# Optimization experiments

Measured on AMD Instinct MI355X. Metric: run time of the kernel, lower is better.

Reference implementation:

```python
import jax, jax.numpy as jnp
import numpy as np

M = 16
N = 16
T = 100
H1 = (M + N) * 10 * 8          # 2560
H2 = (M * N) * 1 * 4           # 1024
HID = (N * N + M * M) * 10     # 5120, GRU hidden dim


def setup_inputs() -> dict:
    key = jax.random.key(0)
    ks = jax.random.split(key, 16)
    def rn(k, shape, scale=1.0):
        return (jax.random.normal(k, shape, dtype=jnp.float32) * scale)
    inp = {}
    inp["y"] = rn(ks[0], (N, T))
    # scale F so spectral radius ~0.8 -> stable over T steps
    inp["F"] = rn(ks[1], (M, M), 0.2)
    inp["H"] = rn(ks[2], (N, M))
    inp["m1_0"] = rn(ks[3], (M, 1))
    inp["h0"] = rn(ks[4], (HID,))
    D_in, D_out = M + N, M * N
    inp["W1"] = rn(ks[5], (H1, D_in), 1.0 / np.sqrt(D_in))
    inp["b1"] = jnp.zeros((H1,), jnp.float32)
    inp["W_ih"] = rn(ks[6], (3 * HID, H1), 1.0 / np.sqrt(H1))
    inp["b_ih"] = jnp.zeros((3 * HID,), jnp.float32)
    inp["W_hh"] = rn(ks[7], (3 * HID, HID), 1.0 / np.sqrt(HID))
    inp["b_hh"] = jnp.zeros((3 * HID,), jnp.float32)
    inp["W2"] = rn(ks[8], (H2, HID), 1.0 / np.sqrt(HID))
    inp["b2"] = jnp.zeros((H2,), jnp.float32)
    inp["W3"] = rn(ks[9], (D_out, H2), 1.0 / np.sqrt(H2))
    inp["b3"] = jnp.zeros((D_out,), jnp.float32)
    return inp


def _l2_normalize(x):
    # torch F.normalize(p=2, eps=1e-12): x / max(||x||_2, eps)
    return x / jnp.maximum(jnp.linalg.norm(x), 1e-12)


def reference(y, F, H, m1_0, h0, W1, b1, W_ih, b_ih, W_hh, b_hh, W2, b2, W3, b3):
    m, n = F.shape[0], H.shape[0]

    def gru_cell(x, h):
        gi = W_ih @ x + b_ih            # [3*HID]
        gh = W_hh @ h + b_hh            # [3*HID]
        i_r, i_z, i_n = jnp.split(gi, 3)
        h_r, h_z, h_n = jnp.split(gh, 3)
        r = jax.nn.sigmoid(i_r + h_r)
        z = jax.nn.sigmoid(i_z + h_z)
        nn_ = jnp.tanh(i_n + r * h_n)
        return (1.0 - z) * nn_ + z * h

    def step(carry, y_t):
        post, sp_post, h = carry
        # step_prior
        m1x_prior = F @ post            # [m,1]
        m1y = H @ m1x_prior             # [n,1]
        sp_prior = F @ sp_post          # [m,1]
        obs0 = H @ sp_prior             # [n,1]
        # step_KGain_est
        d_norm = _l2_normalize((post - sp_post)[:, 0])
        y_norm = _l2_normalize(y_t - obs0[:, 0])
        kin = jnp.concatenate([d_norm, y_norm])  # [m+n]
        l1 = jax.nn.relu(W1 @ kin + b1)
        h_new = gru_cell(l1, h)
        l2 = jax.nn.relu(W2 @ h_new + b2)
        KG = (W3 @ l2 + b3).reshape(m, n)
        # innovation update
        dy = y_t[:, None] - m1y         # [n,1]
        post_new = m1x_prior + KG @ dy  # [m,1]
        return (post_new, sp_prior, h_new), post_new[:, 0]

    (_, _, _), xs = jax.lax.scan(step, (m1_0, m1_0, h0), y.T)
    return xs.T                         # [m,T]
```

## Files before the change

kernel.cpp:

```cpp
#include <hip/hip_runtime.h>
#include <math.h>

#define Tt  100
#define H1  2560
#define HID 5120
#define H2  1024

enum {
  OFF_POST = 0,
  OFF_SP   = 16,
  OFF_M1X  = 32,
  OFF_M1Y  = 48,
  OFF_SPR  = 64,
  OFF_KIN  = 80,
  OFF_L1   = 112,
  OFF_L2   = 2672,
  OFF_KG   = 3696,
  OFF_HA   = 3952,
  OFF_HB   = 9072,
};

__global__ void k_init(const float* __restrict__ m1_0, const float* __restrict__ h0,
                       float* __restrict__ ws) {
  int i = blockIdx.x * blockDim.x + threadIdx.x;
  if (i < 16) { ws[OFF_POST + i] = m1_0[i]; ws[OFF_SP + i] = m1_0[i]; }
  if (i < HID) ws[OFF_HA + i] = h0[i];
}

__global__ void k_small(const float* __restrict__ Fm, const float* __restrict__ Hm,
                        const float* __restrict__ y, float* __restrict__ ws,
                        float* __restrict__ out, int t, int do_F) {
  __shared__ float s_post[16], s_sp[16], s_m1x[16], s_spr[16], s_d[16], s_yv[16], s_dy[16];
  const int tid = threadIdx.x;
  float* post = ws + OFF_POST;
  float* sp   = ws + OFF_SP;
  float* m1x  = ws + OFF_M1X;
  float* m1y  = ws + OFF_M1Y;
  float* spr  = ws + OFF_SPR;
  float* kin  = ws + OFF_KIN;
  const float* KG = ws + OFF_KG;

  if (do_F) {
    if (tid < 16) s_dy[tid] = y[tid * Tt + (t - 1)] - m1y[tid];
    __syncthreads();
    if (tid < 16) {
      float acc = m1x[tid];
      #pragma unroll
      for (int j = 0; j < 16; j++) acc = fmaf(KG[tid * 16 + j], s_dy[j], acc);
      post[tid] = acc; s_post[tid] = acc;
      out[tid * Tt + (t - 1)] = acc;
      float sv = spr[tid];
      sp[tid] = sv; s_sp[tid] = sv;
    }
    __syncthreads();
  } else {
    if (tid < 16) { s_post[tid] = post[tid]; s_sp[tid] = sp[tid]; }
    __syncthreads();
  }
  if (t >= Tt) return;

  if (tid < 16) {
    float a = 0.f, b = 0.f;
    #pragma unroll
    for (int j = 0; j < 16; j++) {
      a = fmaf(Fm[tid * 16 + j], s_post[j], a);
      b = fmaf(Fm[tid * 16 + j], s_sp[j], b);
    }
    s_m1x[tid] = a; s_spr[tid] = b;
    m1x[tid] = a; spr[tid] = b;
  }
  __syncthreads();
  if (tid < 16) {
    float my = 0.f, ob = 0.f;
    #pragma unroll
    for (int j = 0; j < 16; j++) {
      my = fmaf(Hm[tid * 16 + j], s_m1x[j], my);
      ob = fmaf(Hm[tid * 16 + j], s_spr[j], ob);
    }
    m1y[tid] = my;
    s_yv[tid] = y[tid * Tt + t] - ob;
    s_d[tid] = s_post[tid] - s_sp[tid];
  }
  __syncthreads();
  if (tid < 16) {
    float nd = 0.f, ny = 0.f;
    #pragma unroll
    for (int j = 0; j < 16; j++) { nd += s_d[j] * s_d[j]; ny += s_yv[j] * s_yv[j]; }
    nd = fmaxf(sqrtf(nd), 1e-12f);
    ny = fmaxf(sqrtf(ny), 1e-12f);
    kin[tid]      = s_d[tid] / nd;
    kin[16 + tid] = s_yv[tid] / ny;
  }
}

__global__ void k_l1(const float* __restrict__ W1, const float* __restrict__ b1,
                     const float* __restrict__ kin, float* __restrict__ l1) {
  __shared__ float s_kin[32];
  const int tid = threadIdx.x;
  const int r = blockIdx.x * 256 + tid;
  if (tid < 32) s_kin[tid] = kin[tid];
  __syncthreads();
  const float4* row = (const float4*)(W1 + (size_t)r * 32);
  float acc = b1[r];
  #pragma unroll
  for (int j = 0; j < 8; j++) {
    float4 w = row[j];
    acc = fmaf(w.x, s_kin[4 * j + 0], acc);
    acc = fmaf(w.y, s_kin[4 * j + 1], acc);
    acc = fmaf(w.z, s_kin[4 * j + 2], acc);
    acc = fmaf(w.w, s_kin[4 * j + 3], acc);
  }
  l1[r] = fmaxf(acc, 0.f);
}

__device__ __forceinline__ float block_reduce_256(float v, float* sdata) {
  const int tid = threadIdx.x;
  #pragma unroll
  for (int off = 32; off > 0; off >>= 1) v += __shfl_down(v, off, 64);
  __syncthreads();
  if ((tid & 63) == 0) sdata[tid >> 6] = v;
  __syncthreads();
  float r = (tid < 4) ? sdata[tid] : 0.f;
  r += __shfl_down(r, 2, 64);
  r += __shfl_down(r, 1, 64);
  return r;
}

__global__ void k_gru(const float* __restrict__ W_ih, const float* __restrict__ b_ih,
                      const float* __restrict__ W_hh, const float* __restrict__ b_hh,
                      const float* __restrict__ l1, const float* __restrict__ h_in,
                      float* __restrict__ h_out) {
  const int i = blockIdx.x;
  const int tid = threadIdx.x;
  __shared__ float sdata[4];
  const float4* l1v = (const float4*)l1;
  const float4* hv  = (const float4*)h_in;
  float p[6];
  #pragma unroll
  for (int g = 0; g < 3; g++) {
    const float4* row = (const float4*)(W_ih + (size_t)(i + g * HID) * H1);
    float acc = 0.f;
    for (int j = tid; j < H1 / 4; j += 256) {
      float4 w = row[j], x = l1v[j];
      acc = fmaf(w.x, x.x, fmaf(w.y, x.y, fmaf(w.z, x.z, fmaf(w.w, x.w, acc))));
    }
    p[g] = acc;
  }
  #pragma unroll
  for (int g = 0; g < 3; g++) {
    const float4* row = (const float4*)(W_hh + (size_t)(i + g * HID) * HID);
    float acc = 0.f;
    for (int j = tid; j < HID / 4; j += 256) {
      float4 w = row[j], x = hv[j];
      acc = fmaf(w.x, x.x, fmaf(w.y, x.y, fmaf(w.z, x.z, fmaf(w.w, x.w, acc))));
    }
    p[3 + g] = acc;
  }
  float s[6];
  #pragma unroll
  for (int k = 0; k < 6; k++) s[k] = block_reduce_256(p[k], sdata);
  if (tid == 0) {
    float ir = s[0] + b_ih[i], iz = s[1] + b_ih[i + HID], inn = s[2] + b_ih[i + 2 * HID];
    float hr = s[3] + b_hh[i], hz = s[4] + b_hh[i + HID], hn  = s[5] + b_hh[i + 2 * HID];
    float r = 1.f / (1.f + expf(-(ir + hr)));
    float z = 1.f / (1.f + expf(-(iz + hz)));
    float nn = tanhf(inn + r * hn);
    h_out[i] = (1.f - z) * nn + z * h_in[i];
  }
}

__global__ void k_l2(const float* __restrict__ W2, const float* __restrict__ b2,
                     const float* __restrict__ h, float* __restrict__ l2) {
  const int j = blockIdx.x;
  const int tid = threadIdx.x;
  __shared__ float sdata[4];
  const float4* row = (const float4*)(W2 + (size_t)j * HID);
  const float4* xv  = (const float4*)h;
  float acc = 0.f;
  for (int k = tid; k < HID / 4; k += 256) {
    float4 w = row[k], x = xv[k];
    acc = fmaf(w.x, x.x, fmaf(w.y, x.y, fmaf(w.z, x.z, fmaf(w.w, x.w, acc))));
  }
  float s = block_reduce_256(acc, sdata);
  if (tid == 0) l2[j] = fmaxf(s + b2[j], 0.f);
}

__global__ void k_kg(const float* __restrict__ W3, const float* __restrict__ b3,
                     const float* __restrict__ l2, float* __restrict__ KG) {
  const int k = blockIdx.x;
  const int tid = threadIdx.x;
  const float4* row = (const float4*)(W3 + (size_t)k * H2);
  const float4* xv  = (const float4*)l2;
  float acc = 0.f;
  for (int j = tid; j < H2 / 4; j += 64) {
    float4 w = row[j], x = xv[j];
    acc = fmaf(w.x, x.x, fmaf(w.y, x.y, fmaf(w.z, x.z, fmaf(w.w, x.w, acc))));
  }
  #pragma unroll
  for (int off = 32; off > 0; off >>= 1) acc += __shfl_down(acc, off, 64);
  if (tid == 0) KG[k] = acc + b3[k];
}

extern "C" void kernel_launch(void* const* d_in, const int* in_sizes, int n_in,
                              void* d_out, int out_size, void* d_ws, size_t ws_size,
                              hipStream_t stream) {
  const float* y    = (const float*)d_in[0];
  const float* Fm   = (const float*)d_in[1];
  const float* Hm   = (const float*)d_in[2];
  const float* m1_0 = (const float*)d_in[3];
  const float* h0   = (const float*)d_in[4];
  const float* W1   = (const float*)d_in[5];
  const float* b1   = (const float*)d_in[6];
  const float* W_ih = (const float*)d_in[7];
  const float* b_ih = (const float*)d_in[8];
  const float* W_hh = (const float*)d_in[9];
  const float* b_hh = (const float*)d_in[10];
  const float* W2   = (const float*)d_in[11];
  const float* b2   = (const float*)d_in[12];
  const float* W3   = (const float*)d_in[13];
  const float* b3   = (const float*)d_in[14];
  float* out = (float*)d_out;
  float* ws  = (float*)d_ws;

  k_init<<<(HID + 255) / 256, 256, 0, stream>>>(m1_0, h0, ws);

  for (int t = 0; t < Tt; t++) {
    k_small<<<1, 64, 0, stream>>>(Fm, Hm, y, ws, out, t, t > 0 ? 1 : 0);
    k_l1<<<H1 / 256, 256, 0, stream>>>(W1, b1, ws + OFF_KIN, ws + OFF_L1);
    const float* h_in = ws + ((t & 1) ? OFF_HB : OFF_HA);
    float* h_out      = ws + ((t & 1) ? OFF_HA : OFF_HB);
    k_gru<<<HID, 256, 0, stream>>>(W_ih, b_ih, W_hh, b_hh, ws + OFF_L1, h_in, h_out);
    k_l2<<<H2, 256, 0, stream>>>(W2, b2, h_out, ws + OFF_L2);
    k_kg<<<256, 64, 0, stream>>>(W3, b3, ws + OFF_L2, ws + OFF_KG);
  }
  k_small<<<1, 64, 0, stream>>>(Fm, Hm, y, ws, out, Tt, 1);
}
```

Before: 10.84 ms.

## Replace per-timestep kernel launches with single persistent kernel using atomic flag barriers

Folds the 100-step loop of five kernel launches into one persistent kernel of 1024 blocks. The blocks synchronise through atomic epoch counters and flags in workspace, and each block handles five GRU rows. The W_hh matvec is issued before waiting for l1, so it overlaps with block 0's serial Kalman and layer-1 work, and weight streams use nontemporal loads. The aim is to remove launch overhead and inter-kernel gaps. In exchange, correctness depends on all 1024 blocks being co-resident to avoid deadlock, and the spin-waits carry a bounded timeout.

```diff
diff --git a/kernel.cpp b/kernel.cpp
--- a/kernel.cpp
+++ b/kernel.cpp
@@ -5,200 +5,303 @@
 #define H1  2560
 #define HID 5120
 #define H2  1024
-
-enum {
-  OFF_POST = 0,
-  OFF_SP   = 16,
-  OFF_M1X  = 32,
-  OFF_M1Y  = 48,
-  OFF_SPR  = 64,
-  OFF_KIN  = 80,
-  OFF_L1   = 112,
-  OFF_L2   = 2672,
-  OFF_KG   = 3696,
-  OFF_HA   = 3952,
-  OFF_HB   = 9072,
-};
-
-__global__ void k_init(const float* __restrict__ m1_0, const float* __restrict__ h0,
-                       float* __restrict__ ws) {
-  int i = blockIdx.x * blockDim.x + threadIdx.x;
-  if (i < 16) { ws[OFF_POST + i] = m1_0[i]; ws[OFF_SP + i] = m1_0[i]; }
-  if (i < HID) ws[OFF_HA + i] = h0[i];
-}
-
-__global__ void k_small(const float* __restrict__ Fm, const float* __restrict__ Hm,
-                        const float* __restrict__ y, float* __restrict__ ws,
-                        float* __restrict__ out, int t, int do_F) {
-  __shared__ float s_post[16], s_sp[16], s_m1x[16], s_spr[16], s_d[16], s_yv[16], s_dy[16];
+#define NB  1024
+#define GPB 5
+
+typedef float v4 __attribute__((ext_vector_type(4)));
+
+#define FI_HEP   0
+#define FI_L1EP  16
+#define FI_L2EP  32
+#define FI_KGEP  48
+#define FI_HCNT  64
+#define FI_L2CNT 80
+#define FI_KGCNT 96
+
+#define OFF_M1X 128
+#define OFF_M1Y 144
+#define OFF_SPR 160
+#define OFF_KG  208
+#define OFF_L2  464
+#define OFF_L1  1488
+#define OFF_HB0 4048
+#define OFF_HB1 9168
+
+__device__ __forceinline__ void wait_ge(int* p, int v) {
+  if (threadIdx.x == 0) {
+    for (long it = 0; it < 10000000L; ++it) {
+      if (__hip_atomic_load(p, __ATOMIC_RELAXED, __HIP_MEMORY_SCOPE_AGENT) >= v) break;
+      __builtin_amdgcn_s_sleep(8);
+    }
+  }
+  __syncthreads();
+  __builtin_amdgcn_fence(__ATOMIC_ACQUIRE, "agent");
+}
+
+__device__ __forceinline__ void arrive(int* cnt, int* ep, int target, int epval) {
+  if (threadIdx.x == 0) {
+    __builtin_amdgcn_fence(__ATOMIC_RELEASE, "agent");
+    int c = __hip_atomic_fetch_add(cnt, 1, __ATOMIC_RELAXED, __HIP_MEMORY_SCOPE_AGENT);
+    if (c == target - 1) {
+      __builtin_amdgcn_fence(__ATOMIC_ACQUIRE, "agent");
+      __hip_atomic_store(ep, epval, __ATOMIC_RELEASE, __HIP_MEMORY_SCOPE_AGENT);
+    }
+  }
+}
+
+__device__ __forceinline__ float dot4(v4 w, v4 x, float acc) {
+  return fmaf(w.x, x.x, fmaf(w.y, x.y, fmaf(w.z, x.z, fmaf(w.w, x.w, acc))));
+}
+
+__global__ void k_pre(const float* __restrict__ m1_0, const float* __restrict__ h0,
+                      const float* __restrict__ y, const float* __restrict__ Fm,
+                      const float* __restrict__ Hm, const float* __restrict__ W1,
+                      const float* __restrict__ b1, float* __restrict__ ws) {
   const int tid = threadIdx.x;
-  float* post = ws + OFF_POST;
-  float* sp   = ws + OFF_SP;
-  float* m1x  = ws + OFF_M1X;
-  float* m1y  = ws + OFF_M1Y;
-  float* spr  = ws + OFF_SPR;
-  float* kin  = ws + OFF_KIN;
-  const float* KG = ws + OFF_KG;
-
-  if (do_F) {
-    if (tid < 16) s_dy[tid] = y[tid * Tt + (t - 1)] - m1y[tid];
-    __syncthreads();
+  __shared__ float s_m1x[16], s_kin[32];
+  __shared__ float s_ny;
+  for (int i = tid; i < HID; i += 256) ws[OFF_HB1 + i] = h0[i];
+  if (tid < 16) {
+    float a = 0.f;
+    #pragma unroll
+    for (int j = 0; j < 16; j++) a = fmaf(Fm[tid * 16 + j], m1_0[j], a);
+    s_m1x[tid] = a;
+  }
+  __syncthreads();
+  if (tid < 16) {
+    float my = 0.f;
+    #pragma unroll
+    for (int j = 0; j < 16; j++) my = fmaf(Hm[tid * 16 + j], s_m1x[j], my);
+    ws[OFF_M1X + tid] = s_m1x[tid];
+    ws[OFF_M1Y + tid] = my;
+    ws[OFF_SPR + tid] = s_m1x[tid];
+    s_kin[16 + tid] = y[tid * Tt + 0] - my;
+  }
+  __syncthreads();
+  if (tid == 0) {
+    float ny = 0.f;
+    #pragma unroll
+    for (int j = 0; j < 16; j++) ny += s_kin[16 + j] * s_kin[16 + j];
+    s_ny = fmaxf(sqrtf(ny), 1e-12f);
+  }
+  __syncthreads();
+  if (tid < 16) {
+    s_kin[tid] = 0.f;
+    s_kin[16 + tid] = s_kin[16 + tid] / s_ny;
+  }
+  __syncthreads();
+  for (int r = tid; r < H1; r += 256) {
+    const v4* row = (const v4*)(W1 + (size_t)r * 32);
+    float acc = b1[r];
+    #pragma unroll
+    for (int j = 0; j < 8; j++) {
+      v4 w = row[j];
+      acc = fmaf(w.x, s_kin[4 * j], fmaf(w.y, s_kin[4 * j + 1],
+            fmaf(w.z, s_kin[4 * j + 2], fmaf(w.w, s_kin[4 * j + 3], acc))));
+    }
+    ws[OFF_L1 + r] = fmaxf(acc, 0.f);
+  }
+  __syncthreads();
+  if (tid == 0) ((int*)ws)[FI_L1EP] = 1;
+}
+
+__launch_bounds__(256, 4)
+__global__ void k_persist(const float* __restrict__ y, const float* __restrict__ Fm,
+                          const float* __restrict__ Hm,
+                          const float* __restrict__ W1, const float* __restrict__ b1,
+                          const float* __restrict__ W_ih, const float* __restrict__ b_ih,
+                          const float* __restrict__ W_hh, const float* __restrict__ b_hh,
+                          const float* __restrict__ W2, const float* __restrict__ b2,
+                          const float* __restrict__ W3, const float* __restrict__ b3,
+                          float* __restrict__ out, float* __restrict__ ws) {
+  const int b = blockIdx.x, tid = threadIdx.x;
+  int* flags = (int*)ws;
+  float* l1  = ws + OFF_L1;
+  float* l2v = ws + OFF_L2;
+  float* KGg = ws + OFF_KG;
+
+  __shared__ float red[4][32];
+  __shared__ float s_m1x[16], s_m1y[16], s_spr[16], s_post[16], s_sp[16];
+  __shared__ float s_dy[16], s_d[16], s_yv[16], s_kin[32], s_nrm[2];
+
+  if (b == 0) {
     if (tid < 16) {
-      float acc = m1x[tid];
+      s_m1x[tid] = ws[OFF_M1X + tid];
+      s_m1y[tid] = ws[OFF_M1Y + tid];
+      s_spr[tid] = ws[OFF_SPR + tid];
+    }
+    __syncthreads();
+  }
+
+  for (int t = 0; t < Tt; ++t) {
+    wait_ge(flags + FI_HEP, t);
+    const float* hp = ws + ((t & 1) ? OFF_HB0 : OFF_HB1);
+    float*       hc = ws + ((t & 1) ? OFF_HB1 : OFF_HB0);
+    const v4* hp4 = (const v4*)hp;
+
+    float pv[30];
+    #pragma unroll
+    for (int k = 0; k < GPB; ++k) {
+      const int i = b + k * NB;
       #pragma unroll
-      for (int j = 0; j < 16; j++) acc = fmaf(KG[tid * 16 + j], s_dy[j], acc);
-      post[tid] = acc; s_post[tid] = acc;
-      out[tid * Tt + (t - 1)] = acc;
-      float sv = spr[tid];
-      sp[tid] = sv; s_sp[tid] = sv;
-    }
-    __syncthreads();
-  } else {
-    if (tid < 16) { s_post[tid] = post[tid]; s_sp[tid] = sp[tid]; }
-    __syncthreads();
-  }
-  if (t >= Tt) return;
-
-  if (tid < 16) {
-    float a = 0.f, b = 0.f;
-    #pragma unroll
-    for (int j = 0; j < 16; j++) {
-      a = fmaf(Fm[tid * 16 + j], s_post[j], a);
-      b = fmaf(Fm[tid * 16 + j], s_sp[j], b);
-    }
-    s_m1x[tid] = a; s_spr[tid] = b;
-    m1x[tid] = a; spr[tid] = b;
-  }
-  __syncthreads();
-  if (tid < 16) {
-    float my = 0.f, ob = 0.f;
-    #pragma unroll
-    for (int j = 0; j < 16; j++) {
-      my = fmaf(Hm[tid * 16 + j], s_m1x[j], my);
-      ob = fmaf(Hm[tid * 16 + j], s_spr[j], ob);
-    }
-    m1y[tid] = my;
-    s_yv[tid] = y[tid * Tt + t] - ob;
-    s_d[tid] = s_post[tid] - s_sp[tid];
-  }
-  __syncthreads();
-  if (tid < 16) {
-    float nd = 0.f, ny = 0.f;
-    #pragma unroll
-    for (int j = 0; j < 16; j++) { nd += s_d[j] * s_d[j]; ny += s_yv[j] * s_yv[j]; }
-    nd = fmaxf(sqrtf(nd), 1e-12f);
-    ny = fmaxf(sqrtf(ny), 1e-12f);
-    kin[tid]      = s_d[tid] / nd;
-    kin[16 + tid] = s_yv[tid] / ny;
-  }
-}
-
-__global__ void k_l1(const float* __restrict__ W1, const float* __restrict__ b1,
-                     const float* __restrict__ kin, float* __restrict__ l1) {
-  __shared__ float s_kin[32];
-  const int tid = threadIdx.x;
-  const int r = blockIdx.x * 256 + tid;
-  if (tid < 32) s_kin[tid] = kin[tid];
-  __syncthreads();
-  const float4* row = (const float4*)(W1 + (size_t)r * 32);
-  float acc = b1[r];
-  #pragma unroll
-  for (int j = 0; j < 8; j++) {
-    float4 w = row[j];
-    acc = fmaf(w.x, s_kin[4 * j + 0], acc);
-    acc = fmaf(w.y, s_kin[4 * j + 1], acc);
-    acc = fmaf(w.z, s_kin[4 * j + 2], acc);
-    acc = fmaf(w.w, s_kin[4 * j + 3], acc);
-  }
-  l1[r] = fmaxf(acc, 0.f);
-}
-
-__device__ __forceinline__ float block_reduce_256(float v, float* sdata) {
-  const int tid = threadIdx.x;
-  #pragma unroll
-  for (int off = 32; off > 0; off >>= 1) v += __shfl_down(v, off, 64);
-  __syncthreads();
-  if ((tid & 63) == 0) sdata[tid >> 6] = v;
-  __syncthreads();
-  float r = (tid < 4) ? sdata[tid] : 0.f;
-  r += __shfl_down(r, 2, 64);
-  r += __shfl_down(r, 1, 64);
-  return r;
-}
-
-__global__ void k_gru(const float* __restrict__ W_ih, const float* __restrict__ b_ih,
-                      const float* __restrict__ W_hh, const float* __restrict__ b_hh,
-                      const float* __restrict__ l1, const float* __restrict__ h_in,
-                      float* __restrict__ h_out) {
-  const int i = blockIdx.x;
-  const int tid = threadIdx.x;
-  __shared__ float sdata[4];
-  const float4* l1v = (const float4*)l1;
-  const float4* hv  = (const float4*)h_in;
-  float p[6];
-  #pragma unroll
-  for (int g = 0; g < 3; g++) {
-    const float4* row = (const float4*)(W_ih + (size_t)(i + g * HID) * H1);
-    float acc = 0.f;
-    for (int j = tid; j < H1 / 4; j += 256) {
-      float4 w = row[j], x = l1v[j];
-      acc = fmaf(w.x, x.x, fmaf(w.y, x.y, fmaf(w.z, x.z, fmaf(w.w, x.w, acc))));
-    }
-    p[g] = acc;
-  }
-  #pragma unroll
-  for (int g = 0; g < 3; g++) {
-    const float4* row = (const float4*)(W_hh + (size_t)(i + g * HID) * HID);
-    float acc = 0.f;
-    for (int j = tid; j < HID / 4; j += 256) {
-      float4 w = row[j], x = hv[j];
-      acc = fmaf(w.x, x.x, fmaf(w.y, x.y, fmaf(w.z, x.z, fmaf(w.w, x.w, acc))));
-    }
-    p[3 + g] = acc;
-  }
-  float s[6];
-  #pragma unroll
-  for (int k = 0; k < 6; k++) s[k] = block_reduce_256(p[k], sdata);
-  if (tid == 0) {
-    float ir = s[0] + b_ih[i], iz = s[1] + b_ih[i + HID], inn = s[2] + b_ih[i + 2 * HID];
-    float hr = s[3] + b_hh[i], hz = s[4] + b_hh[i + HID], hn  = s[5] + b_hh[i + 2 * HID];
-    float r = 1.f / (1.f + expf(-(ir + hr)));
-    float z = 1.f / (1.f + expf(-(iz + hz)));
-    float nn = tanhf(inn + r * hn);
-    h_out[i] = (1.f - z) * nn + z * h_in[i];
-  }
-}
-
-__global__ void k_l2(const float* __restrict__ W2, const float* __restrict__ b2,
-                     const float* __restrict__ h, float* __restrict__ l2) {
-  const int j = blockIdx.x;
-  const int tid = threadIdx.x;
-  __shared__ float sdata[4];
-  const float4* row = (const float4*)(W2 + (size_t)j * HID);
-  const float4* xv  = (const float4*)h;
-  float acc = 0.f;
-  for (int k = tid; k < HID / 4; k += 256) {
-    float4 w = row[k], x = xv[k];
-    acc = fmaf(w.x, x.x, fmaf(w.y, x.y, fmaf(w.z, x.z, fmaf(w.w, x.w, acc))));
-  }
-  float s = block_reduce_256(acc, sdata);
-  if (tid == 0) l2[j] = fmaxf(s + b2[j], 0.f);
-}
-
-__global__ void k_kg(const float* __restrict__ W3, const float* __restrict__ b3,
-                     const float* __restrict__ l2, float* __restrict__ KG) {
-  const int k = blockIdx.x;
-  const int tid = threadIdx.x;
-  const float4* row = (const float4*)(W3 + (size_t)k * H2);
-  const float4* xv  = (const float4*)l2;
-  float acc = 0.f;
-  for (int j = tid; j < H2 / 4; j += 64) {
-    float4 w = row[j], x = xv[j];
-    acc = fmaf(w.x, x.x, fmaf(w.y, x.y, fmaf(w.z, x.z, fmaf(w.w, x.w, acc))));
-  }
-  #pragma unroll
-  for (int off = 32; off > 0; off >>= 1) acc += __shfl_down(acc, off, 64);
-  if (tid == 0) KG[k] = acc + b3[k];
+      for (int g = 0; g < 3; ++g) {
+        const v4* row = (const v4*)(W_hh + (size_t)(i + g * HID) * HID);
+        float acc = 0.f;
+        for (int j = tid; j < HID / 4; j += 256) {
+          v4 w = __builtin_nontemporal_load(&row[j]);
+          acc = dot4(w, hp4[j], acc);
+        }
+        pv[k * 6 + 3 + g] = acc;
+      }
+    }
+    wait_ge(flags + FI_L1EP, t + 1);
+    const v4* l14 = (const v4*)l1;
+    #pragma unroll
+    for (int k = 0; k < GPB; ++k) {
+      const int i = b + k * NB;
+      #pragma unroll
+      for (int g = 0; g < 3; ++g) {
+        const v4* row = (const v4*)(W_ih + (size_t)(i + g * HID) * H1);
+        float acc = 0.f;
+        for (int j = tid; j < H1 / 4; j += 256) {
+          v4 w = __builtin_nontemporal_load(&row[j]);
+          acc = dot4(w, l14[j], acc);
+        }
+        pv[k * 6 + g] = acc;
+      }
+    }
+    __syncthreads();
+    #pragma unroll
+    for (int q = 0; q < 30; ++q) {
+      float v = pv[q];
+      v += __shfl_down(v, 32, 64); v += __shfl_down(v, 16, 64);
+      v += __shfl_down(v, 8, 64);  v += __shfl_down(v, 4, 64);
+      v += __shfl_down(v, 2, 64);  v += __shfl_down(v, 1, 64);
+      pv[q] = v;
+    }
+    if ((tid & 63) == 0) {
+      const int w = tid >> 6;
+      #pragma unroll
+      for (int q = 0; q < 30; ++q) red[w][q] = pv[q];
+    }
+    __syncthreads();
+    if (tid < 30) red[0][tid] = red[0][tid] + red[1][tid] + red[2][tid] + red[3][tid];
+    __syncthreads();
+    if (tid < GPB) {
+      const int i = b + tid * NB;
+      float ir = red[0][tid * 6 + 0] + b_ih[i];
+      float iz = red[0][tid * 6 + 1] + b_ih[i + HID];
+      float in_ = red[0][tid * 6 + 2] + b_ih[i + 2 * HID];
+      float hr = red[0][tid * 6 + 3] + b_hh[i];
+      float hz = red[0][tid * 6 + 4] + b_hh[i + HID];
+      float hn = red[0][tid * 6 + 5] + b_hh[i + 2 * HID];
+      float r  = 1.f / (1.f + expf(-(ir + hr)));
+      float z  = 1.f / (1.f + expf(-(iz + hz)));
+      float nn = tanhf(in_ + r * hn);
+      hc[i] = (1.f - z) * nn + z * hp[i];
+    }
+    __syncthreads();
+    arrive(flags + FI_HCNT, flags + FI_HEP, NB * (t + 1), t + 1);
+
+    wait_ge(flags + FI_HEP, t + 1);
+    {
+      const v4* row = (const v4*)(W2 + (size_t)b * HID);
+      const v4* x4 = (const v4*)hc;
+      float acc = 0.f;
+      for (int j = tid; j < HID / 4; j += 256)
+        acc = dot4(__builtin_nontemporal_load(&row[j]), x4[j], acc);
+      acc += __shfl_down(acc, 32, 64); acc += __shfl_down(acc, 16, 64);
+      acc += __shfl_down(acc, 8, 64);  acc += __shfl_down(acc, 4, 64);
+      acc += __shfl_down(acc, 2, 64);  acc += __shfl_down(acc, 1, 64);
+      if ((tid & 63) == 0) red[tid >> 6][0] = acc;
+      __syncthreads();
+      if (tid == 0)
+        l2v[b] = fmaxf(red[0][0] + red[1][0] + red[2][0] + red[3][0] + b2[b], 0.f);
+      arrive(flags + FI_L2CNT, flags + FI_L2EP, NB * (t + 1), t + 1);
+    }
+    if (b < 256) {
+      wait_ge(flags + FI_L2EP, t + 1);
+      const v4* row = (const v4*)(W3 + (size_t)b * H2);
+      const v4* x4 = (const v4*)l2v;
+      v4 w = row[tid];
+      float acc = dot4(w, x4[tid], 0.f);
+      acc += __shfl_down(acc, 32, 64); acc += __shfl_down(acc, 16, 64);
+      acc += __shfl_down(acc, 8, 64);  acc += __shfl_down(acc, 4, 64);
+      acc += __shfl_down(acc, 2, 64);  acc += __shfl_down(acc, 1, 64);
+      if ((tid & 63) == 0) red[tid >> 6][0] = acc;
+      __syncthreads();
+      if (tid == 0) KGg[b] = red[0][0] + red[1][0] + red[2][0] + red[3][0] + b3[b];
+      arrive(flags + FI_KGCNT, flags + FI_KGEP, 256 * (t + 1), t + 1);
+    }
+    if (b == 0) {
+      wait_ge(flags + FI_KGEP, t + 1);
+      if (tid < 16) s_dy[tid] = y[tid * Tt + t] - s_m1y[tid];
+      __syncthreads();
+      if (tid < 16) {
+        float acc = s_m1x[tid];
+        #pragma unroll
+        for (int j = 0; j < 16; j++) acc = fmaf(KGg[tid * 16 + j], s_dy[j], acc);
+        s_post[tid] = acc;
+        out[tid * Tt + t] = acc;
+        s_sp[tid] = s_spr[tid];
+      }
+      __syncthreads();
+      if (t < Tt - 1) {
+        if (tid < 16) {
+          float a = 0.f, bb = 0.f;
+          #pragma unroll
+          for (int j = 0; j < 16; j++) {
+            a  = fmaf(Fm[tid * 16 + j], s_post[j], a);
+            bb = fmaf(Fm[tid * 16 + j], s_sp[j], bb);
+          }
+          s_m1x[tid] = a; s_spr[tid] = bb;
+        }
+        __syncthreads();
+        if (tid < 16) {
+          float my = 0.f, ob = 0.f;
+          #pragma unroll
+          for (int j = 0; j < 16; j++) {
+            my = fmaf(Hm[tid * 16 + j], s_m1x[j], my);
+            ob = fmaf(Hm[tid * 16 + j], s_spr[j], ob);
+          }
+          s_m1y[tid] = my;
+          s_d[tid] = s_post[tid] - s_sp[tid];
+          s_yv[tid] = y[tid * Tt + (t + 1)] - ob;
+        }
+        __syncthreads();
+        if (tid == 0) {
+          float nd = 0.f, ny = 0.f;
+          #pragma unroll
+          for (int j = 0; j < 16; j++) { nd += s_d[j] * s_d[j]; ny += s_yv[j] * s_yv[j]; }
+          s_nrm[0] = fmaxf(sqrtf(nd), 1e-12f);
+          s_nrm[1] = fmaxf(sqrtf(ny), 1e-12f);
+        }
+        __syncthreads();
+        if (tid < 16) {
+          s_kin[tid] = s_d[tid] / s_nrm[0];
+          s_kin[16 + tid] = s_yv[tid] / s_nrm[1];
+        }
+        __syncthreads();
+        for (int r = tid; r < H1; r += 256) {
+          const v4* row = (const v4*)(W1 + (size_t)r * 32);
+          float acc = b1[r];
+          #pragma unroll
+          for (int j = 0; j < 8; j++) {
+            v4 w = row[j];
+            acc = fmaf(w.x, s_kin[4 * j], fmaf(w.y, s_kin[4 * j + 1],
+                  fmaf(w.z, s_kin[4 * j + 2], fmaf(w.w, s_kin[4 * j + 3], acc))));
+          }
+          l1[r] = fmaxf(acc, 0.f);
+        }
+        __syncthreads();
+        if (tid == 0) {
+          __builtin_amdgcn_fence(__ATOMIC_RELEASE, "agent");
+          __hip_atomic_store(flags + FI_L1EP, t + 2, __ATOMIC_RELEASE,
+                             __HIP_MEMORY_SCOPE_AGENT);
+        }
+      }
+    }
+  }
 }
 
 extern "C" void kernel_launch(void* const* d_in, const int* in_sizes, int n_in,
@@ -222,16 +325,8 @@
   float* out = (float*)d_out;
   float* ws  = (float*)d_ws;
 
-  k_init<<<(HID + 255) / 256, 256, 0, stream>>>(m1_0, h0, ws);
-
-  for (int t = 0; t < Tt; t++) {
-    k_small<<<1, 64, 0, stream>>>(Fm, Hm, y, ws, out, t, t > 0 ? 1 : 0);
-    k_l1<<<H1 / 256, 256, 0, stream>>>(W1, b1, ws + OFF_KIN, ws + OFF_L1);
-    const float* h_in = ws + ((t & 1) ? OFF_HB : OFF_HA);
-    float* h_out      = ws + ((t & 1) ? OFF_HA : OFF_HB);
-    k_gru<<<HID, 256, 0, stream>>>(W_ih, b_ih, W_hh, b_hh, ws + OFF_L1, h_in, h_out);
-    k_l2<<<H2, 256, 0, stream>>>(W2, b2, h_out, ws + OFF_L2);
-    k_kg<<<256, 64, 0, stream>>>(W3, b3, ws + OFF_L2, ws + OFF_KG);
-  }
-  k_small<<<1, 64, 0, stream>>>(Fm, Hm, y, ws, out, Tt, 1);
-}
+  (void)hipMemsetAsync(ws, 0, 512, stream);
+  k_pre<<<1, 256, 0, stream>>>(m1_0, h0, y, Fm, Hm, W1, b1, ws);
+  k_persist<<<NB, 256, 0, stream>>>(y, Fm, Hm, W1, b1, W_ih, b_ih, W_hh, b_hh,
+                                    W2, b2, W3, b3, out, ws);
+}
```

Result: slower. 24.91 ms (+129.9%).
